# Kernel tuning notes

Measured on AMD Instinct MI355X. Metric: run time of the kernel, lower is better.

Reference implementation:

```python
import jax, jax.numpy as jnp
import numpy as np

N, IN, OUT, T = 131072, 256, 256, 8

def setup_inputs() -> dict:
    key = jax.random.key(0)
    k1, k2, k3, k4 = jax.random.split(key, 4)
    x = jax.random.normal(k1, (N, IN), dtype=jnp.float32)
    type_vec = jnp.sort(jax.random.randint(k2, (N,), 0, T, dtype=jnp.int64))
    weight = jax.random.normal(k3, (T, IN, OUT), dtype=jnp.float32) * (1.0 / np.sqrt(IN))
    bias = jax.random.normal(k4, (T, OUT), dtype=jnp.float32) * 0.01
    return {"x": x, "type_vec": type_vec, "weight": weight, "bias": bias}

def reference(x, type_vec, weight, bias):
    # HeteroLinear fused forward: out[i] = x[i] @ weight[type_vec[i]] + bias[type_vec[i]]
    # Loop over the small fixed set of types (T=8); mask-accumulate keeps memory at O(N*OUT).
    num_types = weight.shape[0]
    out = jnp.zeros((x.shape[0], weight.shape[2]), dtype=x.dtype)
    for t in range(num_types):
        mask = (type_vec == t)[:, None]  # [N,1]
        out = out + jnp.where(mask, x @ weight[t] + bias[t], jnp.zeros((), x.dtype))
    return out
```

## Files before the change

### kernel.cpp

```cpp
#include <hip/hip_runtime.h>
#include <hip/hip_bf16.h>


#define NROWS 131072
#define KD 256
#define ND 256
#define RT 32
#define TPB 8
#define BM (RT * TPB)
#define NBLK (NROWS / BM)

typedef __attribute__((ext_vector_type(8))) short short8;
typedef __attribute__((ext_vector_type(4))) float f32x4;
typedef __attribute__((ext_vector_type(4))) float flt4;

typedef __attribute__((address_space(3))) unsigned int lds_u32_t;
typedef __attribute__((address_space(1))) unsigned int glb_u32_t;

__device__ inline unsigned short f2bf(float f) {
    unsigned int u = __float_as_uint(f);
    u += 0x7FFFu + ((u >> 16) & 1u);
    return (unsigned short)(u >> 16);
}

__global__ __launch_bounds__(256) void prep_weights(const float* __restrict__ w,
                                                    unsigned short* __restrict__ wT) {
    __shared__ unsigned short L[8][264];
    const int t  = blockIdx.x >> 5;
    const int k0 = (blockIdx.x & 31) * 8;
    const int tid = threadIdx.x;

    #pragma unroll
    for (int i = 0; i < 2; ++i) {
        int idx = i * 256 + tid;
        int kr  = idx >> 6;
        int nq  = idx & 63;
        const flt4* src = (const flt4*)(w + ((size_t)t * 256 + k0 + kr) * 256);
        flt4 v = src[nq];
        #pragma unroll
        for (int j = 0; j < 4; ++j) L[kr][nq * 4 + j] = f2bf(v[j]);
    }
    __syncthreads();

    int n = tid;
    short8 v;
    #pragma unroll
    for (int j = 0; j < 8; ++j) v[j] = (short)L[j][n];
    *(short8*)(wT + ((size_t)t * 256 + n) * 256 + k0) = v;
}

__global__ __launch_bounds__(512) void hetero_gemm(
        const float* __restrict__ x, const int* __restrict__ tv,
        const unsigned short* __restrict__ wT, const float* __restrict__ bias,
        float* __restrict__ out) {
    __shared__ float A[2][RT * 256];

    const int tid  = threadIdx.x;
    const int lane = tid & 63;
    const int wv   = tid >> 6;
    const int cl   = lane & 15;
    const int kg   = lane >> 4;
    const int s    = cl & 7;
    const int tile0 = blockIdx.x * TPB;

    short8 Wf[8][2];
    f32x4  bv[2];
    int wt = -1;
    auto loadWT = [&](int t) {
        const unsigned short* Wt = wT + (size_t)t * (KD * ND);
        #pragma unroll
        for (int ks = 0; ks < 8; ++ks)
            #pragma unroll
            for (int n = 0; n < 2; ++n)
                Wf[ks][n] = *(const short8*)(Wt + (size_t)(wv * 32 + n * 16 + cl) * KD
                                             + ks * 32 + kg * 8);
        bv[0] = *(const f32x4*)(bias + (size_t)t * ND + wv * 32 + kg * 4);
        bv[1] = *(const f32x4*)(bias + (size_t)t * ND + wv * 32 + 16 + kg * 4);
        wt = t;
    };

    auto stage = [&](int buf, int tile) {
        #pragma unroll
        for (int i = 0; i < 4; ++i) {
            int r = wv * 4 + i;
            const float* gp = x + ((size_t)tile * RT + r) * KD + ((lane ^ (r & 7)) << 2);
            __builtin_amdgcn_global_load_lds((const glb_u32_t*)gp,
                                             (lds_u32_t*)&A[buf][r * 256],
                                             16, 0, 0);
        }
    };

    loadWT(tv[tile0 * RT]);
    stage(0, tile0);
    __syncthreads();

    for (int it = 0; it < TPB; ++it) {
        const int tile = tile0 + it;
        const int r0   = tile * RT;
        if (it + 1 < TPB) stage((it + 1) & 1, tile + 1);

        const int tmin = tv[r0];
        const int tmax = tv[r0 + RT - 1];
        const int ty0  = tv[r0 + cl];
        const int ty1  = tv[r0 + 16 + cl];
        const float* Ab = &A[it & 1][0];

        for (int t = tmin; t <= tmax; ++t) {
            if (t != wt) loadWT(t);

            f32x4 zero = {0.f, 0.f, 0.f, 0.f};
            f32x4 acc[2][2];
            acc[0][0] = zero; acc[0][1] = zero;
            acc[1][0] = zero; acc[1][1] = zero;

            #pragma unroll
            for (int ks = 0; ks < 8; ++ks) {
                short8 a[2];
                #pragma unroll
                for (int m = 0; m < 2; ++m) {
                    const int c0 = ks * 8 + kg * 2;
                    const float* rp = Ab + (m * 16 + cl) * 256;
                    f32x4 v0 = *(const f32x4*)(rp + ((c0 ^ s) << 2));
                    f32x4 v1 = *(const f32x4*)(rp + (((c0 + 1) ^ s) << 2));
                    #pragma unroll
                    for (int j = 0; j < 4; ++j) {
                        a[m][j]     = (short)f2bf(v0[j]);
                        a[m][4 + j] = (short)f2bf(v1[j]);
                    }
                }
                #pragma unroll
                for (int m = 0; m < 2; ++m) {
                    acc[m][0] = __builtin_amdgcn_mfma_f32_16x16x32_bf16(Wf[ks][0], a[m], acc[m][0], 0, 0, 0);
                    acc[m][1] = __builtin_amdgcn_mfma_f32_16x16x32_bf16(Wf[ks][1], a[m], acc[m][1], 0, 0, 0);
                }
            }

            #pragma unroll
            for (int m = 0; m < 2; ++m) {
                int tym = (m == 0) ? ty0 : ty1;
                if (tym == t) {
                    float* orow = out + (size_t)(r0 + m * 16 + cl) * ND + wv * 32 + kg * 4;
                    *(f32x4*)(orow)      = acc[m][0] + bv[0];
                    *(f32x4*)(orow + 16) = acc[m][1] + bv[1];
                }
            }
        }

        __syncthreads();
    }
}

extern "C" void kernel_launch(void* const* d_in, const int* in_sizes, int n_in,
                              void* d_out, int out_size, void* d_ws, size_t ws_size,
                              hipStream_t stream) {
    const float* x    = (const float*)d_in[0];
    const int*   tv   = (const int*)d_in[1];
    const float* w    = (const float*)d_in[2];
    const float* bias = (const float*)d_in[3];
    float* out = (float*)d_out;
    unsigned short* wT = (unsigned short*)d_ws;

    prep_weights<<<dim3(256), dim3(256), 0, stream>>>(w, wT);
    hetero_gemm<<<dim3(NBLK), dim3(512), 0, stream>>>(x, tv, wT, bias, out);
}
```

Baseline: 79.75 us.

## Replace LDS-staged x tiles with direct register loads and split columns across blocks

Drops the LDS double-buffered global_load_lds staging of x and instead has each lane load its x fragments straight from global memory into registers, prefetching the next k-slice. Each block now handles one 32-row tile and half the output columns with 256 threads, giving 8192 blocks instead of 512 multi-tile blocks. This removes LDS traffic and barriers, and raises parallelism. In exchange, every 32-row tile of x is read twice (once per column half) and each block reloads its weight fragments, so there is no reuse across tiles. Global reads are strided per lane, which may hurt coalescing.

```diff
diff --git a/kernel.cpp b/kernel.cpp
--- a/kernel.cpp
+++ b/kernel.cpp
@@ -5,17 +5,12 @@
 #define NROWS 131072
 #define KD 256
 #define ND 256
-#define RT 32
-#define TPB 8
-#define BM (RT * TPB)
-#define NBLK (NROWS / BM)
+#define BR 32
+#define NBLK ((NROWS / BR) * 2)
 
 typedef __attribute__((ext_vector_type(8))) short short8;
 typedef __attribute__((ext_vector_type(4))) float f32x4;
 typedef __attribute__((ext_vector_type(4))) float flt4;
-
-typedef __attribute__((address_space(3))) unsigned int lds_u32_t;
-typedef __attribute__((address_space(1))) unsigned int glb_u32_t;
 
 __device__ inline unsigned short f2bf(float f) {
     unsigned int u = __float_as_uint(f);
@@ -49,22 +44,26 @@
     *(short8*)(wT + ((size_t)t * 256 + n) * 256 + k0) = v;
 }
 
-__global__ __launch_bounds__(512) void hetero_gemm(
+__global__ __launch_bounds__(256) void hetero_gemm(
         const float* __restrict__ x, const int* __restrict__ tv,
         const unsigned short* __restrict__ wT, const float* __restrict__ bias,
         float* __restrict__ out) {
-    __shared__ float A[2][RT * 256];
-
     const int tid  = threadIdx.x;
     const int lane = tid & 63;
     const int wv   = tid >> 6;
     const int cl   = lane & 15;
     const int kg   = lane >> 4;
-    const int s    = cl & 7;
-    const int tile0 = blockIdx.x * TPB;
+    const int rg   = blockIdx.x >> 1;
+    const int cb   = (blockIdx.x & 1) * 128;
+    const int r0   = rg * BR;
+    const int c0   = cb + wv * 32;
+
+    const int tmin = tv[r0];
+    const int tmax = tv[r0 + BR - 1];
+    const int ty0  = tv[r0 + cl];
+    const int ty1  = tv[r0 + 16 + cl];
 
     short8 Wf[8][2];
-    f32x4  bv[2];
     int wt = -1;
     auto loadWT = [&](int t) {
         const unsigned short* Wt = wT + (size_t)t * (KD * ND);
@@ -72,81 +71,66 @@
         for (int ks = 0; ks < 8; ++ks)
             #pragma unroll
             for (int n = 0; n < 2; ++n)
-                Wf[ks][n] = *(const short8*)(Wt + (size_t)(wv * 32 + n * 16 + cl) * KD
+                Wf[ks][n] = *(const short8*)(Wt + (size_t)(c0 + n * 16 + cl) * KD
                                              + ks * 32 + kg * 8);
-        bv[0] = *(const f32x4*)(bias + (size_t)t * ND + wv * 32 + kg * 4);
-        bv[1] = *(const f32x4*)(bias + (size_t)t * ND + wv * 32 + 16 + kg * 4);
         wt = t;
     };
+    loadWT(tmin);
 
-    auto stage = [&](int buf, int tile) {
+    const float* xr0 = x + (size_t)(r0 + cl) * KD + kg * 8;
+    const float* xr1 = x + (size_t)(r0 + 16 + cl) * KD + kg * 8;
+
+    for (int t = tmin; t <= tmax; ++t) {
+        if (t != wt) loadWT(t);
+
+        f32x4 zero = {0.f, 0.f, 0.f, 0.f};
+        f32x4 acc[2][2];
+        acc[0][0] = zero; acc[0][1] = zero;
+        acc[1][0] = zero; acc[1][1] = zero;
+
+        f32x4 xv[4];
+        xv[0] = *(const f32x4*)(xr0);
+        xv[1] = *(const f32x4*)(xr0 + 4);
+        xv[2] = *(const f32x4*)(xr1);
+        xv[3] = *(const f32x4*)(xr1 + 4);
+
         #pragma unroll
-        for (int i = 0; i < 4; ++i) {
-            int r = wv * 4 + i;
-            const float* gp = x + ((size_t)tile * RT + r) * KD + ((lane ^ (r & 7)) << 2);
-            __builtin_amdgcn_global_load_lds((const glb_u32_t*)gp,
-                                             (lds_u32_t*)&A[buf][r * 256],
-                                             16, 0, 0);
-        }
-    };
-
-    loadWT(tv[tile0 * RT]);
-    stage(0, tile0);
-    __syncthreads();
-
-    for (int it = 0; it < TPB; ++it) {
-        const int tile = tile0 + it;
-        const int r0   = tile * RT;
-        if (it + 1 < TPB) stage((it + 1) & 1, tile + 1);
-
-        const int tmin = tv[r0];
-        const int tmax = tv[r0 + RT - 1];
-        const int ty0  = tv[r0 + cl];
-        const int ty1  = tv[r0 + 16 + cl];
-        const float* Ab = &A[it & 1][0];
-
-        for (int t = tmin; t <= tmax; ++t) {
-            if (t != wt) loadWT(t);
-
-            f32x4 zero = {0.f, 0.f, 0.f, 0.f};
-            f32x4 acc[2][2];
-            acc[0][0] = zero; acc[0][1] = zero;
-            acc[1][0] = zero; acc[1][1] = zero;
-
+        for (int ks = 0; ks < 8; ++ks) {
+            f32x4 xn[4];
+            if (ks < 7) {
+                xn[0] = *(const f32x4*)(xr0 + (ks + 1) * 32);
+                xn[1] = *(const f32x4*)(xr0 + (ks + 1) * 32 + 4);
+                xn[2] = *(const f32x4*)(xr1 + (ks + 1) * 32);
+                xn[3] = *(const f32x4*)(xr1 + (ks + 1) * 32 + 4);
+            }
+            short8 a[2];
             #pragma unroll
-            for (int ks = 0; ks < 8; ++ks) {
-                short8 a[2];
+            for (int m = 0; m < 2; ++m) {
                 #pragma unroll
-                for (int m = 0; m < 2; ++m) {
-                    const int c0 = ks * 8 + kg * 2;
-                    const float* rp = Ab + (m * 16 + cl) * 256;
-                    f32x4 v0 = *(const f32x4*)(rp + ((c0 ^ s) << 2));
-                    f32x4 v1 = *(const f32x4*)(rp + (((c0 + 1) ^ s) << 2));
-                    #pragma unroll
-                    for (int j = 0; j < 4; ++j) {
-                        a[m][j]     = (short)f2bf(v0[j]);
-                        a[m][4 + j] = (short)f2bf(v1[j]);
-                    }
-                }
-                #pragma unroll
-                for (int m = 0; m < 2; ++m) {
-                    acc[m][0] = __builtin_amdgcn_mfma_f32_16x16x32_bf16(Wf[ks][0], a[m], acc[m][0], 0, 0, 0);
-                    acc[m][1] = __builtin_amdgcn_mfma_f32_16x16x32_bf16(Wf[ks][1], a[m], acc[m][1], 0, 0, 0);
+                for (int j = 0; j < 4; ++j) {
+                    a[m][j]     = (short)f2bf(xv[2 * m][j]);
+                    a[m][4 + j] = (short)f2bf(xv[2 * m + 1][j]);
                 }
             }
-
             #pragma unroll
             for (int m = 0; m < 2; ++m) {
-                int tym = (m == 0) ? ty0 : ty1;
-                if (tym == t) {
-                    float* orow = out + (size_t)(r0 + m * 16 + cl) * ND + wv * 32 + kg * 4;
-                    *(f32x4*)(orow)      = acc[m][0] + bv[0];
-                    *(f32x4*)(orow + 16) = acc[m][1] + bv[1];
-                }
+                acc[m][0] = __builtin_amdgcn_mfma_f32_16x16x32_bf16(Wf[ks][0], a[m], acc[m][0], 0, 0, 0);
+                acc[m][1] = __builtin_amdgcn_mfma_f32_16x16x32_bf16(Wf[ks][1], a[m], acc[m][1], 0, 0, 0);
+            }
+            xv[0] = xn[0]; xv[1] = xn[1]; xv[2] = xn[2]; xv[3] = xn[3];
+        }
+
+        #pragma unroll
+        for (int m = 0; m < 2; ++m) {
+            int tym = (m == 0) ? ty0 : ty1;
+            if (tym == t) {
+                float* orow = out + (size_t)(r0 + m * 16 + cl) * ND + c0 + kg * 4;
+                f32x4 bv0 = *(const f32x4*)(bias + (size_t)t * ND + c0 + kg * 4);
+                f32x4 bv1 = *(const f32x4*)(bias + (size_t)t * ND + c0 + 16 + kg * 4);
+                *(f32x4*)(orow)      = acc[m][0] + bv0;
+                *(f32x4*)(orow + 16) = acc[m][1] + bv1;
             }
         }
-
-        __syncthreads();
     }
 }
 
@@ -161,5 +145,5 @@
     unsigned short* wT = (unsigned short*)d_ws;
 
     prep_weights<<<dim3(256), dim3(256), 0, stream>>>(w, wT);
-    hetero_gemm<<<dim3(NBLK), dim3(512), 0, stream>>>(x, tv, wT, bias, out);
+    hetero_gemm<<<dim3(NBLK), dim3(256), 0, stream>>>(x, tv, wT, bias, out);
 }
```

Result: slower. 198.4 us (+148.8%).
